# Kernel optimization log

Hardware: AMD Instinct MI355X
Metric: run time of the kernel (lower is better)

Reference implementation:

```python
import jax, jax.numpy as jnp
import numpy as np

EPSILON = 1e-8
K = 3
PAD = K // 2


def setup_inputs() -> dict:
    key = jax.random.key(0)
    k1, k2, k3, k4 = jax.random.split(key, 4)
    B, FI, FO, H, W, DSTYLE = 8, 512, 512, 64, 64, 512
    return {
        "x": jax.random.normal(k1, (B, FI, H, W), dtype=jnp.float32),
        "style": jax.random.normal(k2, (B, DSTYLE), dtype=jnp.float32),
        "w": jax.random.normal(k3, (FO, FI, K, K), dtype=jnp.float32),
        "fc_w": jax.random.normal(k4, (FI, DSTYLE), dtype=jnp.float32),  # modLinear weight [dim_out=fi, dim_in=dim_style]
        "fc_b": jnp.zeros((FI,), dtype=jnp.float32),
    }


def reference(x, style, w, fc_w, fc_b):
    B, FI, H, W = x.shape
    FO = w.shape[0]
    DSTYLE = fc_w.shape[1]
    fc_scale = DSTYLE ** (-0.5)            # modLinear w_scale (lr_mult=1)
    w_scale = (FI * K * K) ** (-0.5)       # modConv w_scale

    # modLinear: style -> per-input-channel modulation s, shape [B, FI]
    s = style @ (fc_w * fc_scale).T + fc_b

    # Demod factor: d[b, fo] = rsqrt(sum_{fi,k,k} (w_scale * w * s[b,fi])^2 + eps)
    wsq = jnp.sum((w * w_scale) ** 2, axis=(2, 3))          # [FO, FI]
    d = jax.lax.rsqrt(jnp.einsum('of,bf->bo', wsq, s ** 2) + EPSILON)  # [B, FO]

    # Equivalent to per-sample grouped conv: scale input channels by s,
    # conv with shared base weight, scale output channels by demod.
    xm = x * s[:, :, None, None]
    y = jax.lax.conv_general_dilated(
        xm, w * w_scale,
        window_strides=(1, 1),
        padding=((PAD, PAD), (PAD, PAD)),
        dimension_numbers=('NCHW', 'OIHW', 'NCHW'),
    )
    return y * d[:, :, None, None]
```

## Files before the change

### kernel.cpp

```cpp
#include <hip/hip_runtime.h>


typedef __bf16 bf16_t;
typedef __bf16 bf16x8 __attribute__((ext_vector_type(8)));
typedef float floatx4 __attribute__((ext_vector_type(4)));

#define HW_ 4096
#define FCSCALE 0.04419417382415922f
#define WSCALE  0.014731391274719742f

#define VMCNT(n) asm volatile("s_waitcnt vmcnt(" #n ")" ::: "memory")

__device__ __forceinline__ void gload_lds16(const bf16_t* g, bf16_t* l) {
  __builtin_amdgcn_global_load_lds(
      (const __attribute__((address_space(1))) void*)g,
      (__attribute__((address_space(3))) void*)l, 16, 0, 0);
}


__device__ __forceinline__ void style_body(int bid, int t,
    const float* __restrict__ style, const float* __restrict__ fc_w,
    const float* __restrict__ fc_b, float* __restrict__ s_out) {
  int o = bid * 4 + (t >> 6);
  int lane = t & 63;
  int b = o >> 9, fi = o & 511;
  const float4* st = (const float4*)(style + b * 512);
  const float4* fw = (const float4*)(fc_w + (size_t)fi * 512);
  float4 a0 = st[lane * 2],     w0 = fw[lane * 2];
  float4 a1 = st[lane * 2 + 1], w1 = fw[lane * 2 + 1];
  float acc = a0.x * w0.x + a0.y * w0.y + a0.z * w0.z + a0.w * w0.w
            + a1.x * w1.x + a1.y * w1.y + a1.z * w1.z + a1.w * w1.w;
#pragma unroll
  for (int d = 32; d >= 1; d >>= 1) acc += __shfl_xor(acc, d, 64);
  if (lane == 0) s_out[o] = acc * FCSCALE + fc_b[fi];
}

__device__ __forceinline__ void wsq_wt_body(int bid, int t,
    const float* __restrict__ w, float* __restrict__ wsq, bf16_t* __restrict__ wt) {
  int idx = bid * 256 + t;
  int fo = idx >> 9, fi = idx & 511;
  const float* wp = w + (size_t)idx * 9;
  float v[9], q = 0.f;
#pragma unroll
  for (int k = 0; k < 9; ++k) { v[k] = wp[k] * WSCALE; q += v[k] * v[k]; }
  wsq[idx] = q;
#pragma unroll
  for (int k = 0; k < 9; ++k)
    wt[((((size_t)k * 64) + (fi >> 3)) * 512 + fo) * 8 + (fi & 7)] = (bf16_t)v[k];
}

__device__ __forceinline__ void demod_body(int bid, int t,
    const float* __restrict__ wsq, const float* __restrict__ s,
    float* __restrict__ dcoef) {
  int o = bid * 4 + (t >> 6);
  int lane = t & 63;
  int b = o >> 9, fo = o & 511;
  const float4* wq = (const float4*)(wsq + (size_t)fo * 512);
  const float4* sp = (const float4*)(s + b * 512);
  float acc = 0.f;
#pragma unroll
  for (int i = 0; i < 2; ++i) {
    float4 q = wq[lane * 2 + i], sv = sp[lane * 2 + i];
    acc += q.x * sv.x * sv.x + q.y * sv.y * sv.y + q.z * sv.z * sv.z + q.w * sv.w * sv.w;
  }
#pragma unroll
  for (int d = 32; d >= 1; d >>= 1) acc += __shfl_xor(acc, d, 64);
  if (lane == 0) dcoef[o] = rsqrtf(acc + 1e-8f);
}

__global__ void k_prep1(const float* __restrict__ style, const float* __restrict__ fc_w,
                        const float* __restrict__ fc_b, const float* __restrict__ w,
                        float* __restrict__ s_out, float* __restrict__ wsq,
                        bf16_t* __restrict__ wt, bf16_t* __restrict__ zerobuf) {
  int blk = blockIdx.x, t = threadIdx.x;
  if (blk < 1024) {
    wsq_wt_body(blk, t, w, wsq, wt);
  } else if (blk < 2048) {
    style_body(blk - 1024, t, style, fc_w, fc_b, s_out);
  } else {
    if (t < 128) zerobuf[t] = (bf16_t)0.f;
  }
}

__device__ __forceinline__ void modx_body(int fi0, int h, int b, int t,
    const float* __restrict__ x, const float* __restrict__ s,
    bf16_t* __restrict__ xT, float (*tile)[65]) {
  int c4 = (t & 15) * 4, fr = t >> 4;
#pragma unroll
  for (int i = 0; i < 2; ++i) {
    int fi_l = i * 16 + fr;
    float sv = s[b * 512 + fi0 + fi_l];
    float4 v = *(const float4*)(x + ((size_t)(b * 512 + fi0 + fi_l)) * HW_ + h * 64 + c4);
    tile[fi_l][c4] = v.x * sv; tile[fi_l][c4 + 1] = v.y * sv;
    tile[fi_l][c4 + 2] = v.z * sv; tile[fi_l][c4 + 3] = v.w * sv;
  }
  __syncthreads();
  int g_l = t >> 6, wcol = t & 63;
  bf16x8 vv;
#pragma unroll
  for (int j = 0; j < 8; ++j) vv[j] = (bf16_t)tile[g_l * 8 + j][wcol];
  *(bf16x8*)&xT[((((size_t)(b * 64 + h)) * 64 + (fi0 >> 3) + g_l) * 64 + wcol) * 8] = vv;
}

__global__ void k_prep2(const float* __restrict__ x, const float* __restrict__ s,
                        const float* __restrict__ wsq, float* __restrict__ dcoef,
                        bf16_t* __restrict__ xT) {
  __shared__ float tile[32][65];
  int blk = blockIdx.x, t = threadIdx.x;
  if (blk < 1024) {
    demod_body(blk, t, wsq, s, dcoef);
  } else {
    int m = blk - 1024;
    int b = m >> 10, rem = m & 1023;
    int h = rem >> 4, fi0 = (rem & 15) * 32;
    modx_body(fi0, h, b, t, x, s, xT, tile);
  }
}

__global__ __launch_bounds__(256, 2) void k_conv(const bf16_t* __restrict__ wt,
                                                 const bf16_t* __restrict__ xT,
                                                 const float* __restrict__ dcoef,
                                                 const bf16_t* __restrict__ zerobuf,
                                                 float* __restrict__ out) {
  __shared__ __align__(16) bf16_t wls[4 * 4 * 128 * 8];

  int b   = blockIdx.x;
  int foB = blockIdx.y;
  int hq  = blockIdx.z;
  int t = threadIdx.x;
  int wv = t >> 6, lane = t & 63, quad = lane >> 4, l16 = lane & 15;
  int h0 = hq * 4;
  int fo_l = t & 127, chunk_hi = t >> 7;

  const bf16_t* xTb = xT + (size_t)b * 64 * 64 * 64 * 8;

  floatx4 acc[8][4];
#pragma unroll
  for (int i = 0; i < 8; ++i)
#pragma unroll
    for (int j = 0; j < 4; ++j) acc[i][j] = (floatx4){0.f, 0.f, 0.f, 0.f};

  auto stage_w = [&](int it, int pf) {
    int gc = (it * 7282) >> 16;
    int tap = it - gc * 9;
    int g0 = gc * 4;
#pragma unroll
    for (int itw = 0; itw < 2; ++itw) {
      int cw = itw * 2 + chunk_hi;
      gload_lds16(wt + ((((size_t)tap * 64) + g0 + cw) * 512 + foB * 128 + fo_l) * 8,
                  &wls[(size_t)pf * 4096 + (itw * 256 + wv * 64) * 8]);
    }
  };

  auto load_x = [&](int it, bf16x8* xf) {
    int gc = (it * 7282) >> 16;
    int tap = it - gc * 9;
    int g0 = gc * 4;
    int kh = tap / 3, kw = tap - kh * 3;
    int rg = h0 + wv + kh - 1;
    bool rok = (unsigned)rg < 64u;
    const bf16_t* rowp = xTb + (((size_t)rg * 64 + g0 + quad) * 64) * 8;
#pragma unroll
    for (int j = 0; j < 4; ++j) {
      int c = j * 16 + l16 + kw - 1;
      const bf16_t* src = (rok && (unsigned)c < 64u) ? rowp + (size_t)c * 8
                                                     : zerobuf;
      xf[j] = *(const bf16x8*)src;
    }
  };

  auto compute = [&](int pc, const bf16x8* xf) {
    const bf16_t* wb = &wls[(size_t)pc * 4096];
    __builtin_amdgcn_s_setprio(1);
#pragma unroll
    for (int i = 0; i < 8; ++i) {
      bf16x8 afr = *(const bf16x8*)&wb[(quad * 128 + i * 16 + l16) * 8];
#pragma unroll
      for (int j = 0; j < 4; ++j)
        acc[i][j] = __builtin_amdgcn_mfma_f32_16x16x32_bf16(afr, xf[j], acc[i][j], 0, 0, 0);
    }
    __builtin_amdgcn_s_setprio(0);
  };

  bf16x8 xfA[4], xfB[4];

  stage_w(0, 0);
  load_x(0, xfA);
  stage_w(1, 1);

  for (int it = 0; it < 140; it += 2) {
    load_x(it + 1, xfB);
    stage_w(it + 2, (it + 2) & 3);
    VMCNT(8);
    __builtin_amdgcn_s_barrier();
    __builtin_amdgcn_sched_barrier(0);
    compute(it & 3, xfA);
    load_x(it + 2, xfA);
    stage_w(it + 3, (it + 3) & 3);
    VMCNT(8);
    __builtin_amdgcn_s_barrier();
    __builtin_amdgcn_sched_barrier(0);
    compute((it + 1) & 3, xfB);
  }
  load_x(141, xfB);
  stage_w(142, 2);
  VMCNT(8);
  __builtin_amdgcn_s_barrier();
  __builtin_amdgcn_sched_barrier(0);
  compute(0, xfA);
  load_x(142, xfA);
  stage_w(143, 3);
  VMCNT(8);
  __builtin_amdgcn_s_barrier();
  __builtin_amdgcn_sched_barrier(0);
  compute(1, xfB);
  load_x(143, xfB);
  VMCNT(6);
  __builtin_amdgcn_s_barrier();
  __builtin_amdgcn_sched_barrier(0);
  compute(2, xfA);
  VMCNT(0);
  __builtin_amdgcn_s_barrier();
  __builtin_amdgcn_sched_barrier(0);
  compute(3, xfB);

  int h = h0 + wv;
#pragma unroll
  for (int i = 0; i < 8; ++i) {
#pragma unroll
    for (int rr = 0; rr < 4; ++rr) {
      int fo_g = foB * 128 + i * 16 + quad * 4 + rr;
      float dm = dcoef[b * 512 + fo_g];
      float* op = out + ((size_t)((b * 512 + fo_g) * 64 + h)) * 64;
#pragma unroll
      for (int j = 0; j < 4; ++j)
        op[j * 16 + l16] = acc[i][j][rr] * dm;
    }
  }
}

extern "C" void kernel_launch(void* const* d_in, const int* in_sizes, int n_in,
                              void* d_out, int out_size, void* d_ws, size_t ws_size,
                              hipStream_t stream) {
  const float* x     = (const float*)d_in[0];
  const float* style = (const float*)d_in[1];
  const float* w     = (const float*)d_in[2];
  const float* fc_w  = (const float*)d_in[3];
  const float* fc_b  = (const float*)d_in[4];
  float* out = (float*)d_out;
  char* ws = (char*)d_ws;

  float*  s       = (float*)(ws);
  float*  dcoef   = (float*)(ws + 16384);
  float*  wsq     = (float*)(ws + 32768);
  bf16_t* zerobuf = (bf16_t*)(ws + 1081344);
  bf16_t* wt      = (bf16_t*)(ws + 1081600);
  bf16_t* xT      = (bf16_t*)(ws + 5800192);

  k_prep1<<<2049, 256, 0, stream>>>(style, fc_w, fc_b, w, s, wsq, wt, zerobuf);
  k_prep2<<<9216, 256, 0, stream>>>(x, s, wsq, dcoef, xT);
  k_conv<<<dim3(8, 4, 16), 256, 0, stream>>>(wt, xT, dcoef, zerobuf, out);
}
```

Measured before the change: 253.2 us.

## Stage input rows in LDS once per channel group and reuse across all nine taps

The conv kernel now loads a 6-row halo tile of the transposed input into LDS once per 32-channel group and reads shifted views from LDS for all 9 kernel taps. Before, every tap reloaded the fragments from global memory, with per-lane bounds checks. Weight staging becomes double-buffered per tap, and the next group's input is double-buffered across phases through a macro-unrolled schedule with explicit vmcnt waits. LDS use grows to about 64KB per block, which may limit occupancy below the two blocks per CU that the launch bounds allow. The added barriers and tight wait counts add synchronisation risk.

```diff
diff --git a/kernel.cpp b/kernel.cpp
--- a/kernel.cpp
+++ b/kernel.cpp
@@ -122,7 +122,7 @@
                                                  const float* __restrict__ dcoef,
                                                  const bf16_t* __restrict__ zerobuf,
                                                  float* __restrict__ out) {
-  __shared__ __align__(16) bf16_t wls[4 * 4 * 128 * 8];
+  __shared__ __align__(16) bf16_t sh[32776];
 
   int b   = blockIdx.x;
   int foB = blockIdx.y;
@@ -133,6 +133,8 @@
   int fo_l = t & 127, chunk_hi = t >> 7;
 
   const bf16_t* xTb = xT + (size_t)b * 64 * 64 * 64 * 8;
+  const bf16_t* zslotp = &sh[32768];
+  int XRB = ((wv * 4 + quad) * 64 + l16) * 8;
 
   floatx4 acc[8][4];
 #pragma unroll
@@ -140,89 +142,110 @@
 #pragma unroll
     for (int j = 0; j < 4; ++j) acc[i][j] = (floatx4){0.f, 0.f, 0.f, 0.f};
 
-  auto stage_w = [&](int it, int pf) {
-    int gc = (it * 7282) >> 16;
-    int tap = it - gc * 9;
-    int g0 = gc * 4;
-#pragma unroll
-    for (int itw = 0; itw < 2; ++itw) {
-      int cw = itw * 2 + chunk_hi;
-      gload_lds16(wt + ((((size_t)tap * 64) + g0 + cw) * 512 + foB * 128 + fo_l) * 8,
-                  &wls[(size_t)pf * 4096 + (itw * 256 + wv * 64) * 8]);
+  if (t < 8) sh[32768 + t] = (bf16_t)0.f;
+#pragma unroll
+  for (int k = 0; k < 3; ++k)
+#pragma unroll
+    for (int u = 0; u < 2; ++u) {
+      int s = k * 8 + wv * 2 + u;
+      int r = s >> 2, g = s & 3;
+      int rg = h0 + r - 1;
+      const bf16_t* src = ((unsigned)rg < 64u)
+          ? xTb + (((size_t)rg * 64 + g) * 64 + lane) * 8
+          : zerobuf;
+      gload_lds16(src, &sh[((r * 4 + g) * 64) * 8]);
     }
-  };
-
-  auto load_x = [&](int it, bf16x8* xf) {
-    int gc = (it * 7282) >> 16;
-    int tap = it - gc * 9;
-    int g0 = gc * 4;
-    int kh = tap / 3, kw = tap - kh * 3;
-    int rg = h0 + wv + kh - 1;
-    bool rok = (unsigned)rg < 64u;
-    const bf16_t* rowp = xTb + (((size_t)rg * 64 + g0 + quad) * 64) * 8;
-#pragma unroll
-    for (int j = 0; j < 4; ++j) {
-      int c = j * 16 + l16 + kw - 1;
-      const bf16_t* src = (rok && (unsigned)c < 64u) ? rowp + (size_t)c * 8
-                                                     : zerobuf;
-      xf[j] = *(const bf16x8*)src;
-    }
-  };
-
-  auto compute = [&](int pc, const bf16x8* xf) {
-    const bf16_t* wb = &wls[(size_t)pc * 4096];
-    __builtin_amdgcn_s_setprio(1);
-#pragma unroll
-    for (int i = 0; i < 8; ++i) {
-      bf16x8 afr = *(const bf16x8*)&wb[(quad * 128 + i * 16 + l16) * 8];
-#pragma unroll
-      for (int j = 0; j < 4; ++j)
-        acc[i][j] = __builtin_amdgcn_mfma_f32_16x16x32_bf16(afr, xf[j], acc[i][j], 0, 0, 0);
-    }
-    __builtin_amdgcn_s_setprio(0);
-  };
-
-  bf16x8 xfA[4], xfB[4];
-
-  stage_w(0, 0);
-  load_x(0, xfA);
-  stage_w(1, 1);
-
-  for (int it = 0; it < 140; it += 2) {
-    load_x(it + 1, xfB);
-    stage_w(it + 2, (it + 2) & 3);
-    VMCNT(8);
-    __builtin_amdgcn_s_barrier();
-    __builtin_amdgcn_sched_barrier(0);
-    compute(it & 3, xfA);
-    load_x(it + 2, xfA);
-    stage_w(it + 3, (it + 3) & 3);
-    VMCNT(8);
-    __builtin_amdgcn_s_barrier();
-    __builtin_amdgcn_sched_barrier(0);
-    compute((it + 1) & 3, xfB);
-  }
-  load_x(141, xfB);
-  stage_w(142, 2);
-  VMCNT(8);
-  __builtin_amdgcn_s_barrier();
-  __builtin_amdgcn_sched_barrier(0);
-  compute(0, xfA);
-  load_x(142, xfA);
-  stage_w(143, 3);
-  VMCNT(8);
-  __builtin_amdgcn_s_barrier();
-  __builtin_amdgcn_sched_barrier(0);
-  compute(1, xfB);
-  load_x(143, xfB);
-  VMCNT(6);
-  __builtin_amdgcn_s_barrier();
-  __builtin_amdgcn_sched_barrier(0);
-  compute(2, xfA);
+#pragma unroll
+  for (int itw = 0; itw < 2; ++itw) {
+    int cw = itw * 2 + chunk_hi;
+    gload_lds16(wt + (((size_t)cw) * 512 + foB * 128 + fo_l) * 8,
+                &sh[24576 + (itw * 256 + wv * 64) * 8]);
+  }
   VMCNT(0);
-  __builtin_amdgcn_s_barrier();
-  __builtin_amdgcn_sched_barrier(0);
-  compute(3, xfB);
+  __syncthreads();
+
+#define PHASE(P, NW, XPART, GCLAST)                                            \
+  do {                                                                         \
+    VMCNT(NW);                                                                 \
+    __builtin_amdgcn_s_barrier();                                              \
+    __builtin_amdgcn_sched_barrier(0);                                         \
+    if (!(GCLAST) || (P) < 8) {        \
+      const int TAP1 = ((P) + 1) % 9;                                          \
+      int g01 = ((P) == 8) ? (gc + 1) * 4 : gc * 4;                            \
+      int wb1 = ((gc9 + (P) + 1) & 1) * 4096;                                  \
+      _Pragma("unroll")                                                        \
+      for (int itw = 0; itw < 2; ++itw) {                                      \
+        int cw = itw * 2 + chunk_hi;                                           \
+        gload_lds16(wt + ((((size_t)TAP1 * 64) + g01 + cw) * 512               \
+                          + foB * 128 + fo_l) * 8,                             \
+                    &sh[24576 + wb1 + (itw * 256 + wv * 64) * 8]);             \
+      }                                                                        \
+    }                                                                          \
+    if ((XPART) >= 0 && !(GCLAST)) { \
+      int xb1 = ((gc + 1) & 1) * 12288;                                        \
+      int g0n = (gc + 1) * 4;                                                  \
+      _Pragma("unroll")                                                        \
+      for (int u = 0; u < 2; ++u) {                                            \
+        int s = (XPART) * 8 + wv * 2 + u;                                      \
+        int r = s >> 2, g = s & 3;                                             \
+        int rg = h0 + r - 1;                                                   \
+        const bf16_t* src = ((unsigned)rg < 64u)                               \
+            ? xTb + (((size_t)rg * 64 + g0n + g) * 64 + lane) * 8              \
+            : zerobuf;                                                         \
+        gload_lds16(src, &sh[xb1 + ((r * 4 + g) * 64) * 8]);                   \
+      }                                                                        \
+    }                                                                          \
+    {                                  \
+      const int KH = (P) / 3, KW = (P) % 3;                                    \
+      int xb = (gc & 1) * 12288;                                               \
+      int wb = ((gc9 + (P)) & 1) * 4096;                                       \
+      bf16x8 bfr[4];                                                           \
+      _Pragma("unroll")                                                        \
+      for (int j = 0; j < 4; ++j) {                                            \
+        const bf16_t* ap = &sh[xb + XRB + KH * 2048 + (j * 16 + KW - 1) * 8];  \
+        if (KW == 0 && (j) == 0) { if (l16 == 0)  ap = zslotp; }               \
+        if (KW == 2 && (j) == 3) { if (l16 == 15) ap = zslotp; }               \
+        bfr[j] = *(const bf16x8*)ap;                                           \
+      }                                                                        \
+      __builtin_amdgcn_s_setprio(1);                                           \
+      _Pragma("unroll")                                                        \
+      for (int i = 0; i < 8; ++i) {                                            \
+        bf16x8 afr = *(const bf16x8*)&sh[24576 + wb                            \
+                                         + (quad * 128 + i * 16 + l16) * 8];   \
+        _Pragma("unroll")                                                      \
+        for (int j = 0; j < 4; ++j)                                            \
+          acc[i][j] = __builtin_amdgcn_mfma_f32_16x16x32_bf16(                 \
+              afr, bfr[j], acc[i][j], 0, 0, 0);                                \
+      }                                                                        \
+      __builtin_amdgcn_s_setprio(0);                                           \
+    }                                                                          \
+  } while (0)
+
+  for (int gc = 0; gc < 15; ++gc) {
+    int gc9 = gc * 9;
+    PHASE(0, 0, -1, false);
+    PHASE(1, 0,  0, false);
+    PHASE(2, 2,  1, false);
+    PHASE(3, 2,  2, false);
+    PHASE(4, 2, -1, false);
+    PHASE(5, 0, -1, false);
+    PHASE(6, 0, -1, false);
+    PHASE(7, 0, -1, false);
+    PHASE(8, 0, -1, false);
+  }
+  {
+    int gc = 15, gc9 = 135;
+    PHASE(0, 0, -1, true);
+    PHASE(1, 0, -1, true);
+    PHASE(2, 0, -1, true);
+    PHASE(3, 0, -1, true);
+    PHASE(4, 0, -1, true);
+    PHASE(5, 0, -1, true);
+    PHASE(6, 0, -1, true);
+    PHASE(7, 0, -1, true);
+    PHASE(8, 0, -1, true);
+  }
+#undef PHASE
 
   int h = h0 + wv;
 #pragma unroll
```

Result: faster. 235.4 us (-7.0%).
